# Optimization experiments

Measured on AMD Instinct MI355X. Metric: run time of the kernel, lower is better.

Reference implementation:

```python
import jax, jax.numpy as jnp
import numpy as np

MIN_NORM = 1e-15
C = 1.0            # Poincare ball curvature (geoopt default c=1.0)
SQRT_C = C ** 0.5
EPS_PROJ = 4e-3    # geoopt float32 ball projection epsilon
KERNEL = 3


def _project(x):
    # geoopt PoincareBall projx: clip points to radius (1-eps)/sqrt(c)
    norm = jnp.maximum(jnp.linalg.norm(x, axis=-1, keepdims=True), MIN_NORM)
    maxnorm = (1.0 - EPS_PROJ) / SQRT_C
    return jnp.where(norm > maxnorm, x / norm * maxnorm, x)


def _expmap0(u):
    u_norm = jnp.maximum(jnp.linalg.norm(u, axis=-1, keepdims=True), MIN_NORM)
    gamma = jnp.tanh(jnp.clip(SQRT_C * u_norm, -15.0, 15.0)) * u / (SQRT_C * u_norm)
    return _project(gamma)


def setup_inputs() -> dict:
    key = jax.random.key(0)
    k1, k2, k3 = jax.random.split(key, 3)
    M, B, D, O = 27000, 16, 64, 128  # M = 30^3 voxel positions
    x = jax.random.normal(k1, (M, B, D), dtype=jnp.float32) * 0.3
    # keep points strictly inside the Poincare ball
    n = jnp.linalg.norm(x, axis=-1, keepdims=True)
    x = x * (0.8 * jnp.tanh(n) / jnp.maximum(n, 1e-6))
    # kaiming_normal_(a=sqrt(5)) on (O, D): std = sqrt(2/(1+5))/sqrt(fan_in)
    std = (2.0 / 6.0) ** 0.5 / D ** 0.5
    weight_v = jax.random.normal(k2, (O, D), dtype=jnp.float32) * std
    bound = 4.0 / D ** 0.5
    bias_b = jax.random.uniform(k3, (O, 1), dtype=jnp.float32, minval=-bound, maxval=bound)
    return {"x": x, "weight_v": weight_v, "bias_b": bias_b}


def _gyroplane_conv(x, weight_v, bias_b):
    # x: [sampled_dim=M, batch=B, manifold_dim=D]
    M, B, D = x.shape
    O = weight_v.shape[0]
    N = int(round(M ** (1.0 / 3.0)))
    s = KERNEL // 2
    grid = jnp.transpose(x, (1, 0, 2)).reshape(B, N, N, N, D)
    grid = jnp.pad(grid, ((0, 0), (s, s), (s, s), (s, s), (0, 0)))  # zero pad (origin of ball)
    Np = N + 2 * s
    xp = grid.reshape(B, Np ** 3, D)

    # gyroplane parameters (RiemannianLayer properties)
    p = _expmap0(weight_v * bias_b)                       # bias point on ball, (O, D)
    p2 = jnp.sum(p * p, axis=-1)                          # (O,)
    a = weight_v * jnp.maximum(1.0 - C * p2, MIN_NORM)[:, None]  # transp0(p, _weight), (O, D)

    # normdist2plane(x, p, a, signed=True): diff = mobius_add(-p, x)
    # mobius_add(-p, x) = [alpha*(-p) + beta*x] / den  with
    #   alpha = 1 - 2c<p,x> + c|x|^2, beta = 1 - c|p|^2,
    #   den   = 1 - 2c<p,x> + c^2 |p|^2 |x|^2
    # expand dot products to avoid materializing (B, Mp, O, D)
    x2 = jnp.sum(xp * xp, axis=-1)                        # (B, Mp)
    xdotp = jnp.einsum('bmd,od->bmo', xp, p)              # (B, Mp, O)
    xdota = jnp.einsum('bmd,od->bmo', xp, a)              # (B, Mp, O)
    pa = jnp.sum(p * a, axis=-1)                          # (O,)

    alpha = 1.0 - 2.0 * C * xdotp + C * x2[..., None]
    beta = 1.0 - C * p2                                   # (O,)
    den = jnp.maximum(1.0 - 2.0 * C * xdotp + (C * C) * p2 * x2[..., None], MIN_NORM)

    sc_diff_a = (-alpha * pa + beta * xdota) / den        # <diff, a>, signed
    diff_norm2 = jnp.maximum(
        (alpha * alpha * p2 - 2.0 * alpha * beta * xdotp + beta * beta * x2[..., None]) / (den * den),
        MIN_NORM)
    a_norm = jnp.maximum(jnp.sqrt(jnp.sum(a * a, axis=-1)), MIN_NORM)  # (O,)

    num = 2.0 * SQRT_C * sc_diff_a
    denom = jnp.maximum((1.0 - C * diff_norm2) * a_norm, MIN_NORM)
    dist = jnp.arcsinh(num / denom) / SQRT_C              # (B, Mp, O)

    # sum of per-point distances over each 3x3x3 patch == box filter
    dist = dist.reshape(B, Np, Np, Np, O)
    out = jnp.zeros((B, N, N, N, O), dist.dtype)
    for di in range(KERNEL):
        for dj in range(KERNEL):
            for dk in range(KERNEL):
                out = out + dist[:, di:di + N, dj:dj + N, dk:dk + N, :]
    return jnp.transpose(out, (0, 4, 1, 2, 3))            # (B, O, N, N, N)


def reference(x, weight_v, bias_b):
    return _gyroplane_conv(x, weight_v, bias_b)
```

## Files before the change

### kernel.cpp

```cpp
#include <hip/hip_runtime.h>
#include <math.h>

#define NB 16
#define NO 128
#define ND 64
#define NN 30
#define NM 27000
#define PROW 32
#define PPLANE 960
#define PML 28800

typedef _Float16 half8 __attribute__((ext_vector_type(8)));
typedef _Float16 half4 __attribute__((ext_vector_type(4)));
typedef float    f32x4 __attribute__((ext_vector_type(4)));

__device__ __forceinline__ float asinh_fast(float t) {
    return __logf(t + __builtin_amdgcn_sqrtf(t * t + 1.0f));
}

__device__ __forceinline__ float gyro_dist(float x2, float dp, float da,
                                           float p2, float pa, float an) {
    float beta  = 1.0f - p2;
    float alpha = 1.0f - 2.0f * dp + x2;
    float den   = fmaxf(1.0f - 2.0f * dp + p2 * x2, 1e-15f);
    float rden  = __builtin_amdgcn_rcpf(den);
    float sc    = (beta * da - alpha * pa) * rden;
    float dn2   = fmaxf((alpha * alpha * p2 - 2.0f * alpha * beta * dp +
                         beta * beta * x2) * (rden * rden), 1e-15f);
    float denom = fmaxf((1.0f - dn2) * an, 1e-15f);
    float t     = 2.0f * sc * __builtin_amdgcn_rcpf(denom);
    return asinh_fast(t);
}

__device__ __forceinline__ void param_scalars(float S, float bb,
                                              float* fp_o, float* p2_o,
                                              float* betaC_o, float* pa_o,
                                              float* an_o) {
    float sq  = sqrtf(S);
    float un  = fmaxf(fabsf(bb) * sq, 1e-15f);
    float t1  = tanhf(fminf(un, 15.0f));
    float sc1 = t1 / un;
    float gn  = fmaxf(t1, 1e-15f);
    float sc2 = (gn > 0.996f) ? (0.996f / gn) : 1.0f;
    float fp  = bb * sc1 * sc2;
    float p2  = fp * fp * S;
    float betaC = fmaxf(1.0f - p2, 1e-15f);
    *fp_o = fp; *p2_o = p2; *betaC_o = betaC;
    *pa_o = fp * betaC * S;
    *an_o = fmaxf(betaC * sq, 1e-15f);
}

__device__ __forceinline__ void dist0_wave(const float* __restrict__ w,
                                           const float* __restrict__ bias,
                                           int o, int tid, float* out_lds) {
    if (tid < 64) {
        float v = w[o * ND + tid];
        float s = v * v;
#pragma unroll
        for (int off = 32; off > 0; off >>= 1) s += __shfl_xor(s, off, 64);
        if (tid == 0) {
            float fp, p2, betaC, pa, an;
            param_scalars(s, bias[o], &fp, &p2, &betaC, &pa, &an);
            float dn2   = fmaxf(p2, 1e-15f);
            float denom = fmaxf((1.0f - dn2) * an, 1e-15f);
            *out_lds = asinh_fast(-2.0f * pa * __builtin_amdgcn_rcpf(denom));
        }
    }
}

__global__ __launch_bounds__(128) void gyro_params_k(
    const float* __restrict__ w, const float* __restrict__ bias,
    _Float16* __restrict__ pfg, _Float16* __restrict__ afg,
    float* __restrict__ p2g, float* __restrict__ pag,
    float* __restrict__ ang) {
    int o = threadIdx.x;
    const float* wr = w + o * ND;
    float bb = bias[o];
    float S = 0.0f;
    for (int d = 0; d < ND; ++d) S += wr[d] * wr[d];
    float fp, p2, betaC, pa, an;
    param_scalars(S, bb, &fp, &p2, &betaC, &pa, &an);
    p2g[o] = p2; pag[o] = pa; ang[o] = an;

    half8* pf8 = (half8*)pfg;
    half8* af8 = (half8*)afg;
    int ot8 = o >> 4, j = o & 15;
#pragma unroll
    for (int h = 0; h < 2; ++h)
#pragma unroll
        for (int q = 0; q < 4; ++q) {
            int d0i = h * 32 + q * 8;
            half8 hp, ha;
#pragma unroll
            for (int jj = 0; jj < 8; ++jj) {
                float wv = wr[d0i + jj];
                hp[jj] = (_Float16)(wv * fp);
                ha[jj] = (_Float16)(wv * betaC);
            }
            pf8[(ot8 * 2 + h) * 64 + j + 16 * q] = hp;
            af8[(ot8 * 2 + h) * 64 + j + 16 * q] = ha;
        }
}

__global__ __launch_bounds__(256) void gyro_dist_mfma_h(
    const float* __restrict__ x,
    const _Float16* __restrict__ pfg, const _Float16* __restrict__ afg,
    const float* __restrict__ p2g, const float* __restrict__ pag,
    const float* __restrict__ ang,
    _Float16* __restrict__ tmp) {
    __shared__ __align__(16) half8 xf[8 * 64];
    __shared__ float x2p[64 * 8];
    __shared__ __align__(16) float x2_s[64];

    const int tid = threadIdx.x;
    const int mp0 = blockIdx.x * 64;
    const int b   = blockIdx.y;
    const int lane = tid & 63, wid = tid >> 6;

    const half8* pf8 = (const half8*)pfg;
    const half8* af8 = (const half8*)afg;
    half8 bp[2][2], ba[2][2];
#pragma unroll
    for (int ot = 0; ot < 2; ++ot)
#pragma unroll
        for (int h = 0; h < 2; ++h) {
            int idx = ((wid * 2 + ot) * 2 + h) * 64 + lane;
            bp[ot][h] = pf8[idx];
            ba[ot][h] = af8[idx];
        }

#pragma unroll
    for (int n = 0; n < 2; ++n) {
        int s = tid + n * 256;
        int f = s >> 6, l = s & 63;
        int mt = f >> 1, h = f & 1;
        int mloc = mt * 16 + (l & 15);
        int quad = l >> 4;
        int k0 = h * 32 + quad * 8;
        int gmp = mp0 + mloc;
        int kcol = gmp & 31;
        int row  = gmp >> 5;
        half8 hv;
        float part = 0.0f;
        if (kcol < 30) {
            int gm = row * 30 + kcol;
            const float4* src = (const float4*)(x + ((size_t)gm * NB + b) * ND + k0);
            float4 v0 = src[0], v1 = src[1];
            float vv[8] = {v0.x, v0.y, v0.z, v0.w, v1.x, v1.y, v1.z, v1.w};
#pragma unroll
            for (int jj = 0; jj < 8; ++jj) {
                hv[jj] = (_Float16)vv[jj];
                part += vv[jj] * vv[jj];
            }
        } else {
#pragma unroll
            for (int jj = 0; jj < 8; ++jj) hv[jj] = (_Float16)0.0f;
        }
        xf[f * 64 + l] = hv;
        x2p[mloc * 8 + h * 4 + quad] = part;
    }
    __syncthreads();
    if (tid < 64) {
        float s = 0.0f;
#pragma unroll
        for (int r = 0; r < 8; ++r) s += x2p[tid * 8 + r];
        x2_s[tid] = s;
    }
    __syncthreads();

    f32x4 accp[4][2], acca[4][2];
#pragma unroll
    for (int mt = 0; mt < 4; ++mt)
#pragma unroll
        for (int ot = 0; ot < 2; ++ot) {
            accp[mt][ot] = (f32x4)0.0f;
            acca[mt][ot] = (f32x4)0.0f;
        }
#pragma unroll
    for (int h = 0; h < 2; ++h) {
        half8 afr[4];
#pragma unroll
        for (int mt = 0; mt < 4; ++mt) afr[mt] = xf[(mt * 2 + h) * 64 + lane];
#pragma unroll
        for (int mt = 0; mt < 4; ++mt)
#pragma unroll
            for (int ot = 0; ot < 2; ++ot) {
                accp[mt][ot] = __builtin_amdgcn_mfma_f32_16x16x32_f16(
                    afr[mt], bp[ot][h], accp[mt][ot], 0, 0, 0);
                acca[mt][ot] = __builtin_amdgcn_mfma_f32_16x16x32_f16(
                    afr[mt], ba[ot][h], acca[mt][ot], 0, 0, 0);
            }
    }

    const int lo = lane & 15, quad = lane >> 4;
#pragma unroll
    for (int mt = 0; mt < 4; ++mt)
#pragma unroll
        for (int ot = 0; ot < 2; ++ot) {
            int o   = wid * 32 + ot * 16 + lo;
            int mb  = mt * 16 + quad * 4;
            int gmp = mp0 + mb;
            float4 x2v = *(const float4*)&x2_s[mb];
            float P2 = p2g[o], PA = pag[o], AN = ang[o];
            half4 hv;
            hv[0] = (_Float16)gyro_dist(x2v.x, accp[mt][ot][0], acca[mt][ot][0], P2, PA, AN);
            hv[1] = (_Float16)gyro_dist(x2v.y, accp[mt][ot][1], acca[mt][ot][1], P2, PA, AN);
            hv[2] = (_Float16)gyro_dist(x2v.z, accp[mt][ot][2], acca[mt][ot][2], P2, PA, AN);
            hv[3] = (_Float16)gyro_dist(x2v.w, accp[mt][ot][3], acca[mt][ot][3], P2, PA, AN);
            *(half4*)(tmp + ((size_t)(b * NO + o)) * PML + gmp) = hv;
        }
}

__global__ __launch_bounds__(256) void gyro_box3d_h(
    const _Float16* __restrict__ tmp, float* __restrict__ dst,
    const float* __restrict__ w, const float* __restrict__ bias) {
    __shared__ __align__(16) float vin[10 * PPLANE];
    __shared__ float d0sh;

    const int tid = threadIdx.x;
    const int i0  = blockIdx.x * 8;
    const int o   = blockIdx.y;
    const int b   = blockIdx.z;
    const int bo  = b * NO + o;

    dist0_wave(w, bias, o, tid, &d0sh);
    __syncthreads();
    const float d0 = d0sh;
    float4* vin4 = (float4*)vin;

    const half8* tsrc = (const half8*)(tmp + (size_t)bo * PML);
    for (int idx = tid; idx < 1200; idx += 256) {
        int sl = idx / 120, r8 = idx - sl * 120;
        int ip = i0 - 1 + sl;
        float f[8];
        if (ip >= 0 && ip < NN) {
            half8 hv = tsrc[ip * 120 + r8];
#pragma unroll
            for (int jj = 0; jj < 8; ++jj) f[jj] = (float)hv[jj];
        } else {
#pragma unroll
            for (int jj = 0; jj < 8; ++jj) f[jj] = d0;
        }
        int o4 = (sl * PPLANE + r8 * 8) >> 2;
        float4 v0; v0.x = f[0]; v0.y = f[1]; v0.z = f[2]; v0.w = f[3];
        float4 v1; v1.x = f[4]; v1.y = f[5]; v1.z = f[6]; v1.w = f[7];
        vin4[o4] = v0; vin4[o4 + 1] = v1;
    }
    __syncthreads();

    float4 st[10];

#pragma unroll
    for (int n = 0; n < 10; ++n) {
        int q = tid + n * 256;
        float4 cc, s;
        if (q < 2400) cc = vin4[q];
        float left  = __shfl_up(cc.w, 1);
        float right = __shfl_down(cc.x, 1);
        if (q < 2400) {
            if ((q & 7) == 0) left = d0;
            s.x = left + cc.x + cc.y;
            s.y = cc.x + cc.y + cc.z;
            s.z = cc.y + cc.z + cc.w;
            s.w = cc.z + cc.w + right;
            st[n] = s;
        }
    }
    __syncthreads();
#pragma unroll
    for (int n = 0; n < 10; ++n) {
        int q = tid + n * 256;
        if (q < 2400) vin4[q] = st[n];
    }
    __syncthreads();

    const float T3 = 3.0f * d0;
#pragma unroll
    for (int n = 0; n < 10; ++n) {
        int q = tid + n * 256;
        if (q < 2400) {
            int rem = q % 240;
            int j = rem >> 3;
            float4 cc = vin4[q];
            float4 up, dn;
            if (j == 0)  { up.x = T3; up.y = T3; up.z = T3; up.w = T3; }
            else         up = vin4[q - 8];
            if (j == 29) { dn.x = T3; dn.y = T3; dn.z = T3; dn.w = T3; }
            else         dn = vin4[q + 8];
            float4 s;
            s.x = cc.x + up.x + dn.x; s.y = cc.y + up.y + dn.y;
            s.z = cc.z + up.z + dn.z; s.w = cc.w + up.w + dn.w;
            st[n] = s;
        }
    }
    __syncthreads();
#pragma unroll
    for (int n = 0; n < 10; ++n) {
        int q = tid + n * 256;
        if (q < 2400) vin4[q] = st[n];
    }
    __syncthreads();

    const int nout = (NN - i0 < 8) ? (NN - i0) : 8;
    for (int q = tid; q < nout * 240; q += 256) {
        int pl = q / 240, rem = q - pl * 240;
        int j = rem >> 3, c = rem & 7;
        int o4 = (pl + 1) * 240 + rem;
        float4 a = vin4[o4 - 240], m = vin4[o4], e = vin4[o4 + 240];
        float4 s;
        s.x = a.x + m.x + e.x; s.y = a.y + m.y + e.y;
        s.z = a.z + m.z + e.z; s.w = a.w + m.w + e.w;
        int i = i0 + pl;
        float* g = dst + (size_t)bo * NM + i * 900 + j * 30 + c * 4;
        float2 lo2; lo2.x = s.x; lo2.y = s.y;
        *(float2*)g = lo2;
        if (c < 7) {
            float2 hi2; hi2.x = s.z; hi2.y = s.w;
            *(float2*)(g + 2) = hi2;
        }
    }
}

extern "C" void kernel_launch(void* const* d_in, const int* in_sizes, int n_in,
                              void* d_out, int out_size, void* d_ws, size_t ws_size,
                              hipStream_t stream) {
    const float* x    = (const float*)d_in[0];
    const float* w    = (const float*)d_in[1];
    const float* bias = (const float*)d_in[2];
    float* out = (float*)d_out;

    _Float16* pfg = (_Float16*)d_ws;
    _Float16* afg = (_Float16*)((char*)d_ws + 16384);
    float* p2g = (float*)((char*)d_ws + 32768);
    float* pag = (float*)((char*)d_ws + 33280);
    float* ang = (float*)((char*)d_ws + 33792);
    _Float16* tmp = (_Float16*)((char*)d_ws + 36864);

    gyro_params_k<<<1, 128, 0, stream>>>(w, bias, pfg, afg, p2g, pag, ang);

    dim3 gD(PML / 64, NB);
    gyro_dist_mfma_h<<<gD, 256, 0, stream>>>(x, pfg, afg, p2g, pag, ang, tmp);

    dim3 gB(4, NO, NB);
    gyro_box3d_h<<<gB, 256, 0, stream>>>(tmp, out, w, bias);
}
```

Before: 438.2 us.

## Fuse the innermost-axis box-sum into the distance kernel epilogue via lane shuffles

The first pass of the 3-tap box filter along the innermost spatial axis moves out of the box kernel and into the MFMA distance kernel's epilogue. Neighbouring distances are exchanged with cross-lane shuffles and each row edge is filled with the precomputed origin-distance value. The box kernel drops one shared-memory pass and two barriers, and pads out-of-range planes with three times the origin value. This relies on the MFMA output tile matching contiguous 32-wide rows, and the partial sums are now stored as fp16, which adds rounding of slightly larger values.

After: 438.3 us. No clear change (+0.0%).

```diff
diff --git a/kernel.cpp b/kernel.cpp
--- a/kernel.cpp
+++ b/kernel.cpp
@@ -193,22 +193,45 @@
     }
 
     const int lo = lane & 15, quad = lane >> 4;
-#pragma unroll
-    for (int mt = 0; mt < 4; ++mt)
-#pragma unroll
-        for (int ot = 0; ot < 2; ++ot) {
-            int o   = wid * 32 + ot * 16 + lo;
-            int mb  = mt * 16 + quad * 4;
-            int gmp = mp0 + mb;
+    const size_t obase = (size_t)(b * NO) * PML;
+#pragma unroll
+    for (int ot = 0; ot < 2; ++ot) {
+        const int o = wid * 32 + ot * 16 + lo;
+        const float P2 = p2g[o], PA = pag[o], AN = ang[o];
+        const float denom0 = fmaxf((1.0f - fmaxf(P2, 1e-15f)) * AN, 1e-15f);
+        const float d0 = asinh_fast(-2.0f * PA * __builtin_amdgcn_rcpf(denom0));
+        float dv[4][4];
+#pragma unroll
+        for (int mt = 0; mt < 4; ++mt) {
+            const int mb = mt * 16 + quad * 4;
             float4 x2v = *(const float4*)&x2_s[mb];
-            float P2 = p2g[o], PA = pag[o], AN = ang[o];
+            dv[mt][0] = gyro_dist(x2v.x, accp[mt][ot][0], acca[mt][ot][0], P2, PA, AN);
+            dv[mt][1] = gyro_dist(x2v.y, accp[mt][ot][1], acca[mt][ot][1], P2, PA, AN);
+            dv[mt][2] = gyro_dist(x2v.z, accp[mt][ot][2], acca[mt][ot][2], P2, PA, AN);
+            dv[mt][3] = gyro_dist(x2v.w, accp[mt][ot][3], acca[mt][ot][3], P2, PA, AN);
+        }
+#pragma unroll
+        for (int mt = 0; mt < 4; ++mt) {
+            float tl = __shfl_up(dv[mt][3], 16);
+            float tr = __shfl_down(dv[mt][0], 16);
+            float L, R;
+            if (mt & 1) {
+                float tl2 = __shfl_down(dv[mt - 1][3], 48);
+                L = (quad == 0) ? tl2 : tl;
+                R = (quad == 3) ? d0 : tr;
+            } else {
+                float tr2 = __shfl_up(dv[mt + 1][0], 48);
+                L = (quad == 0) ? d0 : tl;
+                R = (quad == 3) ? tr2 : tr;
+            }
             half4 hv;
-            hv[0] = (_Float16)gyro_dist(x2v.x, accp[mt][ot][0], acca[mt][ot][0], P2, PA, AN);
-            hv[1] = (_Float16)gyro_dist(x2v.y, accp[mt][ot][1], acca[mt][ot][1], P2, PA, AN);
-            hv[2] = (_Float16)gyro_dist(x2v.z, accp[mt][ot][2], acca[mt][ot][2], P2, PA, AN);
-            hv[3] = (_Float16)gyro_dist(x2v.w, accp[mt][ot][3], acca[mt][ot][3], P2, PA, AN);
-            *(half4*)(tmp + ((size_t)(b * NO + o)) * PML + gmp) = hv;
-        }
+            hv[0] = (_Float16)(L + dv[mt][0] + dv[mt][1]);
+            hv[1] = (_Float16)(dv[mt][0] + dv[mt][1] + dv[mt][2]);
+            hv[2] = (_Float16)(dv[mt][1] + dv[mt][2] + dv[mt][3]);
+            hv[3] = (_Float16)(dv[mt][2] + dv[mt][3] + R);
+            *(half4*)(tmp + obase + (size_t)o * PML + (mp0 + mt * 16 + quad * 4)) = hv;
+        }
+    }
 }
 
 __global__ __launch_bounds__(256) void gyro_box3d_h(
@@ -226,6 +249,7 @@
     dist0_wave(w, bias, o, tid, &d0sh);
     __syncthreads();
     const float d0 = d0sh;
+    const float T3 = 3.0f * d0;
     float4* vin4 = (float4*)vin;
 
     const half8* tsrc = (const half8*)(tmp + (size_t)bo * PML);
@@ -239,7 +263,7 @@
             for (int jj = 0; jj < 8; ++jj) f[jj] = (float)hv[jj];
         } else {
 #pragma unroll
-            for (int jj = 0; jj < 8; ++jj) f[jj] = d0;
+            for (int jj = 0; jj < 8; ++jj) f[jj] = T3;
         }
         int o4 = (sl * PPLANE + r8 * 8) >> 2;
         float4 v0; v0.x = f[0]; v0.y = f[1]; v0.z = f[2]; v0.w = f[3];
@@ -250,31 +274,6 @@
 
     float4 st[10];
 
-#pragma unroll
-    for (int n = 0; n < 10; ++n) {
-        int q = tid + n * 256;
-        float4 cc, s;
-        if (q < 2400) cc = vin4[q];
-        float left  = __shfl_up(cc.w, 1);
-        float right = __shfl_down(cc.x, 1);
-        if (q < 2400) {
-            if ((q & 7) == 0) left = d0;
-            s.x = left + cc.x + cc.y;
-            s.y = cc.x + cc.y + cc.z;
-            s.z = cc.y + cc.z + cc.w;
-            s.w = cc.z + cc.w + right;
-            st[n] = s;
-        }
-    }
-    __syncthreads();
-#pragma unroll
-    for (int n = 0; n < 10; ++n) {
-        int q = tid + n * 256;
-        if (q < 2400) vin4[q] = st[n];
-    }
-    __syncthreads();
-
-    const float T3 = 3.0f * d0;
 #pragma unroll
     for (int n = 0; n < 10; ++n) {
         int q = tid + n * 256;
```
